# Optimization experiments

Measured on AMD Instinct MI355X. Metric: run time of the kernel, lower is better.

## Reference

```python
import jax, jax.numpy as jnp
import numpy as np

B, T = 64, 512
VOCAB, E, H = 20, 64, 128
D = 2 * H            # 256, bidirectional LSTM output dim
NH, KD = 8, D // 8   # 8 heads, key_dim 32
DU, OUT = 256, 128
NEG = -1e9


def _lstm_scan(x, mask, W, U, b):
    # x: [B,T,E], mask: [B,T] bool. Keras gate order: i, f, g(c), o.
    Bb = x.shape[0]
    Hh = U.shape[0]
    def step(carry, inp):
        h, c = carry
        xt, mt = inp                      # [B,E], [B]
        z = xt @ W + h @ U + b            # [B,4H]
        i, f, g, o = jnp.split(z, 4, axis=-1)
        c_new = jax.nn.sigmoid(f) * c + jax.nn.sigmoid(i) * jnp.tanh(g)
        h_new = jax.nn.sigmoid(o) * jnp.tanh(c_new)
        m = mt[:, None]
        h = jnp.where(m, h_new, h)        # freeze state/output on masked steps
        c = jnp.where(m, c_new, c)
        return (h, c), h
    h0 = jnp.zeros((Bb, Hh), x.dtype)
    _, ys = jax.lax.scan(step, (h0, h0), (jnp.swapaxes(x, 0, 1), mask.T))
    return jnp.swapaxes(ys, 0, 1)         # [B,T,H]


def setup_inputs() -> dict:
    key = jax.random.key(0)
    ks = jax.random.split(key, 24)
    g = lambda k, shape, s: (jax.random.normal(k, shape, jnp.float32) * s)
    inp = {
        'sequences': jax.random.randint(ks[0], (B, T), 0, VOCAB),
        'emb': g(ks[1], (VOCAB, E), 0.05),
        # forward LSTM
        'Wf': g(ks[2], (E, 4 * H), 0.05), 'Uf': g(ks[3], (H, 4 * H), 0.05), 'bf': jnp.zeros((4 * H,), jnp.float32),
        # backward LSTM
        'Wb': g(ks[4], (E, 4 * H), 0.05), 'Ub': g(ks[5], (H, 4 * H), 0.05), 'bb': jnp.zeros((4 * H,), jnp.float32),
        # MHA projections
        'Wq': g(ks[6], (D, NH, KD), 0.05), 'bq': jnp.zeros((NH, KD), jnp.float32),
        'Wk': g(ks[7], (D, NH, KD), 0.05), 'bk': jnp.zeros((NH, KD), jnp.float32),
        'Wv': g(ks[8], (D, NH, KD), 0.05), 'bv': jnp.zeros((NH, KD), jnp.float32),
        'Wo': g(ks[9], (NH, KD, D), 0.05), 'bo': jnp.zeros((D,), jnp.float32),
        # MLP head (input is concat of avg+max pool -> 2*D)
        'W1': g(ks[10], (2 * D, DU), 0.05), 'b1': jnp.zeros((DU,), jnp.float32),
        'W2': g(ks[11], (DU, DU // 2), 0.05), 'b2': jnp.zeros((DU // 2,), jnp.float32),
        'W3': g(ks[12], (DU // 2, OUT), 0.05), 'b3': jnp.zeros((OUT,), jnp.float32),
    }
    return inp


def _forward(sequences, emb, Wf, Uf, bf, Wb, Ub, bb, Wq, bq, Wk, bk, Wv, bv, Wo, bo, W1, b1, W2, b2, W3, b3):
    mask = sequences != 0                       # mask_zero=True
    x = emb[sequences]                          # [B,T,E]
    fwd = _lstm_scan(x, mask, Wf, Uf, bf)
    bwd = _lstm_scan(x[:, ::-1], mask[:, ::-1], Wb, Ub, bb)[:, ::-1]
    h = jnp.concatenate([fwd, bwd], axis=-1)    # [B,T,D]
    # Multi-head self-attention (key-masked, Keras MHA math)
    q = jnp.einsum('btd,dhk->bthk', h, Wq) + bq
    k = jnp.einsum('btd,dhk->bthk', h, Wk) + bk
    v = jnp.einsum('btd,dhk->bthk', h, Wv) + bv
    scores = jnp.einsum('bthk,bshk->bhts', q, k) / jnp.sqrt(jnp.float32(KD))
    scores = jnp.where(mask[:, None, None, :], scores, NEG)
    attn = jax.nn.softmax(scores, axis=-1)      # [B,H,T,T]
    ctx = jnp.einsum('bhts,bshk->bthk', attn, v)
    att = jnp.einsum('bthk,hkd->btd', ctx, Wo) + bo   # [B,T,D]
    # dual pooling (masked mean + masked max)
    mf = mask[..., None].astype(att.dtype)
    avg = (att * mf).sum(axis=1) / jnp.maximum(mf.sum(axis=1), 1.0)
    mx = jnp.where(mask[..., None], att, NEG).max(axis=1)
    p = jnp.concatenate([avg, mx], axis=-1)     # [B,2D]
    x1 = jax.nn.relu(p @ W1 + b1)
    x2 = jax.nn.relu(x1 @ W2 + b2)
    return x2 @ W3 + b3                         # [B,OUT]


def reference(sequences, emb, Wf, Uf, bf, Wb, Ub, bb, Wq, bq, Wk, bk, Wv, bv, Wo, bo, W1, b1, W2, b2, W3, b3):
    return _forward(sequences, emb, Wf, Uf, bf, Wb, Ub, bb, Wq, bq, Wk, bk, Wv, bv, Wo, bo, W1, b1, W2, b2, W3, b3)
```

## Files before the change

kernel.cpp:

```cpp
#include <hip/hip_runtime.h>
#include <math.h>

#define B_ 64
#define T_ 512
#define E_ 64
#define H_ 128
#define NH_ 8
#define KD_ 32
#define BT_ (B_ * T_)
#define NEG_ -1e9f

__device__ __forceinline__ float sigmoidf_(float x) {
    return 1.f / (1.f + __expf(-x));
}
__device__ __forceinline__ float tanhf_(float x) {
    return 1.f - 2.f / (1.f + __expf(2.f * x));
}

template <bool GATHER>
__global__ __launch_bounds__(256, 3) void gemm_f32(
    const float* __restrict__ A, const int* __restrict__ gidx,
    const float* __restrict__ emb, const float* __restrict__ Bm,
    const float* __restrict__ bias, float* __restrict__ C,
    int M, int N, int K)
{
    __shared__ __align__(16) float As[16][132];
    __shared__ __align__(16) float Bs[16][128];
    const int tid = threadIdx.x;
    const int tx = tid & 15, ty = tid >> 4;
    const int ntn = N >> 7;
    const int bm = blockIdx.x / ntn, bn = blockIdx.x % ntn;
    const int m0 = bm << 7, n0 = bn << 7;

    float acc[8][8];
#pragma unroll
    for (int i = 0; i < 8; ++i)
#pragma unroll
        for (int j = 0; j < 8; ++j) acc[i][j] = 0.f;

    const int ac4 = (tid & 3) << 2;
    const int ar  = tid >> 2;
    const int bc4 = (tid & 31) << 2;
    const int br  = tid >> 5;

    for (int k0 = 0; k0 < K; k0 += 16) {
        __syncthreads();
#pragma unroll
        for (int p = 0; p < 2; ++p) {
            const int r = ar + p * 64;
            const int gm = m0 + r;
            const float* src = GATHER
                ? (emb + (size_t)gidx[gm] * K + (k0 + ac4))
                : (A + (size_t)gm * K + (k0 + ac4));
            float4 v = *(const float4*)src;
            As[ac4 + 0][r] = v.x; As[ac4 + 1][r] = v.y;
            As[ac4 + 2][r] = v.z; As[ac4 + 3][r] = v.w;
        }
#pragma unroll
        for (int p = 0; p < 2; ++p) {
            const int rr = br + p * 8;
            float4 v = *(const float4*)(Bm + (size_t)(k0 + rr) * N + (n0 + bc4));
            *(float4*)&Bs[rr][bc4] = v;
        }
        __syncthreads();
#pragma unroll
        for (int k = 0; k < 16; ++k) {
            float a[8], b[8];
            *(float4*)&a[0] = *(const float4*)&As[k][ty << 3];
            *(float4*)&a[4] = *(const float4*)&As[k][(ty << 3) + 4];
            *(float4*)&b[0] = *(const float4*)&Bs[k][tx << 3];
            *(float4*)&b[4] = *(const float4*)&Bs[k][(tx << 3) + 4];
#pragma unroll
            for (int i = 0; i < 8; ++i)
#pragma unroll
                for (int j = 0; j < 8; ++j)
                    acc[i][j] = fmaf(a[i], b[j], acc[i][j]);
        }
    }

    float bv[8];
#pragma unroll
    for (int j = 0; j < 8; ++j) bv[j] = bias[n0 + (tx << 3) + j];
#pragma unroll
    for (int i = 0; i < 8; ++i) {
        float* dst = C + (size_t)(m0 + (ty << 3) + i) * N + n0 + (tx << 3);
        float4 o0 = { acc[i][0] + bv[0], acc[i][1] + bv[1],
                      acc[i][2] + bv[2], acc[i][3] + bv[3] };
        float4 o1 = { acc[i][4] + bv[4], acc[i][5] + bv[5],
                      acc[i][6] + bv[6], acc[i][7] + bv[7] };
        *(float4*)dst = o0;
        *(float4*)(dst + 4) = o1;
    }
}

__global__ __launch_bounds__(512, 2) void lstm_scan(
    const int* __restrict__ seq,
    const float* __restrict__ xwf, const float* __restrict__ xwb,
    const float* __restrict__ Uf, const float* __restrict__ Ub,
    float* __restrict__ hcat)
{
    const int w = blockIdx.x;
    const int dir = w & 1, b = w >> 1;
    const float* xw = dir ? xwb : xwf;
    const float* U  = dir ? Ub  : Uf;
    const int j = threadIdx.x;

    __shared__ __align__(16) float h_lds[128];
    __shared__ float z_lds[512];

    float u[128];
#pragma unroll
    for (int k = 0; k < 128; ++k) u[k] = U[k * 512 + j];
    if (j < 128) h_lds[j] = 0.f;
    float c_reg = 0.f;

    const int* sq = seq + b * T_;
    const float* xr = xw + (size_t)b * T_ * 512;
    float* ho = hcat + (size_t)b * T_ * 256 + dir * 128;
    __syncthreads();

    for (int t = 0; t < T_; ++t) {
        const int te = dir ? (T_ - 1 - t) : t;
        float a0 = xr[(size_t)te * 512 + j];
        float a1 = 0.f, a2 = 0.f, a3 = 0.f;
#pragma unroll
        for (int k = 0; k < 128; k += 4) {
            float4 h4 = *(const float4*)&h_lds[k];
            a0 = fmaf(h4.x, u[k],     a0);
            a1 = fmaf(h4.y, u[k + 1], a1);
            a2 = fmaf(h4.z, u[k + 2], a2);
            a3 = fmaf(h4.w, u[k + 3], a3);
        }
        const float zv = (a0 + a1) + (a2 + a3);
        const float val = (j >= 256 && j < 384) ? tanhf_(zv) : sigmoidf_(zv);
        z_lds[j] = val;
        __syncthreads();
        if (j < 128) {
            const float iv = z_lds[j], fv = z_lds[128 + j];
            const float gv = z_lds[256 + j], ov = z_lds[384 + j];
            const float cn = fmaf(fv, c_reg, iv * gv);
            const float hn = ov * tanhf_(cn);
            const bool mt = (sq[te] != 0);
            const float hprev = h_lds[j];
            const float hout = mt ? hn : hprev;
            c_reg = mt ? cn : c_reg;
            h_lds[j] = hout;
            ho[(size_t)te * 256 + j] = hout;
        }
        __syncthreads();
    }
}

__global__ __launch_bounds__(256, 2) void attn_fused(
    const int* __restrict__ seq,
    const float* __restrict__ q, const float* __restrict__ kk,
    const float* __restrict__ vv, float* __restrict__ ctx)
{
    const int wg = blockIdx.x;
    const int b = wg >> 3, h = wg & 7;
    const int tid = threadIdx.x;

    __shared__ __align__(16) float Ks[16][32];
    __shared__ __align__(16) float Vs[16][32];
    __shared__ float mk[16];

    float qA[32], qB[32];
    {
        const float* qp  = q + (((size_t)(b * T_) + tid) * NH_ + h) * KD_;
        const float* qp2 = qp + (size_t)256 * NH_ * KD_;
#pragma unroll
        for (int k = 0; k < 32; k += 4) {
            float4 v0 = *(const float4*)(qp + k);
            float4 v1 = *(const float4*)(qp2 + k);
            qA[k] = v0.x; qA[k + 1] = v0.y; qA[k + 2] = v0.z; qA[k + 3] = v0.w;
            qB[k] = v1.x; qB[k + 1] = v1.y; qB[k + 2] = v1.z; qB[k + 3] = v1.w;
        }
    }
    float ctxA[32], ctxB[32];
#pragma unroll
    for (int k = 0; k < 32; ++k) { ctxA[k] = 0.f; ctxB[k] = 0.f; }
    float mA = -1e30f, mB = -1e30f, lA = 0.f, lB = 0.f;

    const int lr = (tid & 127) >> 3;
    const int lc = (tid & 7) << 2;
    const bool loadV = (tid >= 128);

    for (int c = 0; c < T_ / 16; ++c) {
        const int s0 = c << 4;
        __syncthreads();
        {
            const float* src = (loadV ? vv : kk) +
                (((size_t)(b * T_) + s0 + lr) * NH_ + h) * KD_ + lc;
            float4 v = *(const float4*)src;
            if (loadV) *(float4*)&Vs[lr][lc] = v;
            else       *(float4*)&Ks[lr][lc] = v;
            if (tid < 16) mk[tid] = (seq[b * T_ + s0 + tid] != 0) ? 0.f : 1.f;
        }
        __syncthreads();

        float sA[16], sB[16];
#pragma unroll
        for (int s = 0; s < 16; ++s) {
            float dA = 0.f, dB = 0.f;
#pragma unroll
            for (int k = 0; k < 32; k += 4) {
                float4 k4 = *(const float4*)&Ks[s][k];
                dA = fmaf(k4.x, qA[k], dA); dA = fmaf(k4.y, qA[k + 1], dA);
                dA = fmaf(k4.z, qA[k + 2], dA); dA = fmaf(k4.w, qA[k + 3], dA);
                dB = fmaf(k4.x, qB[k], dB); dB = fmaf(k4.y, qB[k + 1], dB);
                dB = fmaf(k4.z, qB[k + 2], dB); dB = fmaf(k4.w, qB[k + 3], dB);
            }
            const float SCL = 0.17677669529663687f;
            const bool masked = (mk[s] > 0.5f);
            sA[s] = masked ? NEG_ : dA * SCL;
            sB[s] = masked ? NEG_ : dB * SCL;
        }
        float cmA = sA[0], cmB = sB[0];
#pragma unroll
        for (int s = 1; s < 16; ++s) {
            cmA = fmaxf(cmA, sA[s]); cmB = fmaxf(cmB, sB[s]);
        }
        const float mnA = fmaxf(mA, cmA), mnB = fmaxf(mB, cmB);
        const float alA = __expf(mA - mnA), alB = __expf(mB - mnB);
        float psA = 0.f, psB = 0.f;
#pragma unroll
        for (int s = 0; s < 16; ++s) {
            float pa = __expf(sA[s] - mnA); sA[s] = pa; psA += pa;
            float pb = __expf(sB[s] - mnB); sB[s] = pb; psB += pb;
        }
        lA = fmaf(lA, alA, psA); lB = fmaf(lB, alB, psB);
        mA = mnA; mB = mnB;
#pragma unroll
        for (int k = 0; k < 32; ++k) { ctxA[k] *= alA; ctxB[k] *= alB; }
#pragma unroll
        for (int s = 0; s < 16; ++s) {
#pragma unroll
            for (int k = 0; k < 32; k += 4) {
                float4 v4 = *(const float4*)&Vs[s][k];
                ctxA[k]     = fmaf(sA[s], v4.x, ctxA[k]);
                ctxA[k + 1] = fmaf(sA[s], v4.y, ctxA[k + 1]);
                ctxA[k + 2] = fmaf(sA[s], v4.z, ctxA[k + 2]);
                ctxA[k + 3] = fmaf(sA[s], v4.w, ctxA[k + 3]);
                ctxB[k]     = fmaf(sB[s], v4.x, ctxB[k]);
                ctxB[k + 1] = fmaf(sB[s], v4.y, ctxB[k + 1]);
                ctxB[k + 2] = fmaf(sB[s], v4.z, ctxB[k + 2]);
                ctxB[k + 3] = fmaf(sB[s], v4.w, ctxB[k + 3]);
            }
        }
    }

    const float iA = 1.f / lA, iB = 1.f / lB;
    float* dA_ = ctx + (((size_t)(b * T_) + tid) * NH_ + h) * KD_;
    float* dB_ = dA_ + (size_t)256 * NH_ * KD_;
#pragma unroll
    for (int k = 0; k < 32; k += 4) {
        float4 o0 = { ctxA[k] * iA, ctxA[k + 1] * iA,
                      ctxA[k + 2] * iA, ctxA[k + 3] * iA };
        float4 o1 = { ctxB[k] * iB, ctxB[k + 1] * iB,
                      ctxB[k + 2] * iB, ctxB[k + 3] * iB };
        *(float4*)(dA_ + k) = o0;
        *(float4*)(dB_ + k) = o1;
    }
}

__global__ void pool_kernel(const int* __restrict__ seq,
                            const float* __restrict__ att,
                            float* __restrict__ p)
{
    const int b = blockIdx.x;
    const int d = threadIdx.x;
    __shared__ float mk[T_];
    for (int t = d; t < T_; t += 256)
        mk[t] = (seq[b * T_ + t] != 0) ? 1.f : 0.f;
    __syncthreads();
    float sum = 0.f, mx = NEG_, cnt = 0.f;
    for (int t = 0; t < T_; ++t) {
        const float a = att[((size_t)b * T_ + t) * 256 + d];
        const float m = mk[t];
        cnt += m;
        sum = fmaf(m, a, sum);
        mx = fmaxf(mx, (m > 0.5f) ? a : NEG_);
    }
    p[b * 512 + d] = sum / fmaxf(cnt, 1.f);
    p[b * 512 + 256 + d] = mx;
}

__global__ void mlp_kernel(const float* __restrict__ p,
                           const float* __restrict__ W1, const float* __restrict__ b1,
                           const float* __restrict__ W2, const float* __restrict__ b2,
                           const float* __restrict__ W3, const float* __restrict__ b3,
                           float* __restrict__ out)
{
    const int b = blockIdx.x;
    const int tid = threadIdx.x;
    __shared__ float pl[512];
    __shared__ float x1l[256];
    __shared__ float x2l[128];
    pl[tid] = p[b * 512 + tid];
    pl[tid + 256] = p[b * 512 + 256 + tid];
    __syncthreads();
    {
        float acc = b1[tid];
        for (int k = 0; k < 512; ++k) acc = fmaf(pl[k], W1[k * 256 + tid], acc);
        x1l[tid] = fmaxf(acc, 0.f);
    }
    __syncthreads();
    if (tid < 128) {
        float acc = b2[tid];
        for (int k = 0; k < 256; ++k) acc = fmaf(x1l[k], W2[k * 128 + tid], acc);
        x2l[tid] = fmaxf(acc, 0.f);
    }
    __syncthreads();
    if (tid < 128) {
        float acc = b3[tid];
        for (int k = 0; k < 128; ++k) acc = fmaf(x2l[k], W3[k * 128 + tid], acc);
        out[b * 128 + tid] = acc;
    }
}

extern "C" void kernel_launch(void* const* d_in, const int* in_sizes, int n_in,
                              void* d_out, int out_size, void* d_ws, size_t ws_size,
                              hipStream_t stream)
{
    (void)in_sizes; (void)n_in; (void)out_size; (void)ws_size;
    const int*   seq = (const int*)d_in[0];
    const float* emb = (const float*)d_in[1];
    const float* Wf  = (const float*)d_in[2];
    const float* Uf  = (const float*)d_in[3];
    const float* bf  = (const float*)d_in[4];
    const float* Wb  = (const float*)d_in[5];
    const float* Ub  = (const float*)d_in[6];
    const float* bb  = (const float*)d_in[7];
    const float* Wq  = (const float*)d_in[8];
    const float* bq  = (const float*)d_in[9];
    const float* Wk  = (const float*)d_in[10];
    const float* bk  = (const float*)d_in[11];
    const float* Wv  = (const float*)d_in[12];
    const float* bv  = (const float*)d_in[13];
    const float* Wo  = (const float*)d_in[14];
    const float* bo  = (const float*)d_in[15];
    const float* W1  = (const float*)d_in[16];
    const float* b1  = (const float*)d_in[17];
    const float* W2  = (const float*)d_in[18];
    const float* b2  = (const float*)d_in[19];
    const float* W3  = (const float*)d_in[20];
    const float* b3  = (const float*)d_in[21];
    float* out = (float*)d_out;
    float* ws  = (float*)d_ws;

    float* xw_f = ws;
    float* xw_b = ws + 16777216;
    float* hcat = ws + 33554432;
    float* qb   = ws;
    float* kb   = ws + 8388608;
    float* vb   = ws + 16777216;
    float* cxb  = ws + 25165824;
    float* attb = ws + 33554432;
    float* pb   = ws + 41943040;

    const dim3 blk256(256), blk512(512);

    gemm_f32<true><<<dim3((BT_ / 128) * (512 / 128)), blk256, 0, stream>>>(
        nullptr, seq, emb, Wf, bf, xw_f, BT_, 512, 64);
    gemm_f32<true><<<dim3((BT_ / 128) * (512 / 128)), blk256, 0, stream>>>(
        nullptr, seq, emb, Wb, bb, xw_b, BT_, 512, 64);

    lstm_scan<<<dim3(128), blk512, 0, stream>>>(seq, xw_f, xw_b, Uf, Ub, hcat);

    gemm_f32<false><<<dim3((BT_ / 128) * (256 / 128)), blk256, 0, stream>>>(
        hcat, nullptr, nullptr, Wq, bq, qb, BT_, 256, 256);
    gemm_f32<false><<<dim3((BT_ / 128) * (256 / 128)), blk256, 0, stream>>>(
        hcat, nullptr, nullptr, Wk, bk, kb, BT_, 256, 256);
    gemm_f32<false><<<dim3((BT_ / 128) * (256 / 128)), blk256, 0, stream>>>(
        hcat, nullptr, nullptr, Wv, bv, vb, BT_, 256, 256);

    attn_fused<<<dim3(B_ * NH_), blk256, 0, stream>>>(seq, qb, kb, vb, cxb);

    gemm_f32<false><<<dim3((BT_ / 128) * (256 / 128)), blk256, 0, stream>>>(
        cxb, nullptr, nullptr, Wo, bo, attb, BT_, 256, 256);

    pool_kernel<<<dim3(B_), blk256, 0, stream>>>(seq, attb, pb);
    mlp_kernel<<<dim3(B_), blk256, 0, stream>>>(pb, W1, b1, W2, b2, W3, b3, out);
}
```

Before: 1.073 ms.

## Restructure LSTM scan with split-K DPP reduction and single barrier per step

The input-projection GEMM now writes gate columns interleaved (i,f,g,o per hidden unit), so each LSTM thread can read all four gate pre-activations for its unit as one float4. The scan assigns 4 threads per hidden unit, each holding a 32-wide K slice of all four gates in registers. Partial sums are reduced with DPP quad swaps, and every thread then computes the cell update redundantly. A double-buffered h in LDS removes the second barrier and the z_lds exchange, and the next step's xw is prefetched one iteration ahead. This targets the per-step latency of the serial recurrence, but it costs strided, uncoalesced B loads in the permuted GEMM.

```diff
diff --git a/kernel.cpp b/kernel.cpp
--- a/kernel.cpp
+++ b/kernel.cpp
@@ -17,7 +17,14 @@
     return 1.f - 2.f / (1.f + __expf(2.f * x));
 }
 
-template <bool GATHER>
+__device__ __forceinline__ float qswap1(float x) {
+    return __int_as_float(__builtin_amdgcn_mov_dpp(__float_as_int(x), 0xB1, 0xF, 0xF, true));
+}
+__device__ __forceinline__ float qswap2(float x) {
+    return __int_as_float(__builtin_amdgcn_mov_dpp(__float_as_int(x), 0x4E, 0xF, 0xF, true));
+}
+
+template <bool GATHER, bool PERM>
 __global__ __launch_bounds__(256, 3) void gemm_f32(
     const float* __restrict__ A, const int* __restrict__ gidx,
     const float* __restrict__ emb, const float* __restrict__ Bm,
@@ -59,8 +66,17 @@
 #pragma unroll
         for (int p = 0; p < 2; ++p) {
             const int rr = br + p * 8;
-            float4 v = *(const float4*)(Bm + (size_t)(k0 + rr) * N + (n0 + bc4));
-            *(float4*)&Bs[rr][bc4] = v;
+            if (PERM) {
+                const float* brow = Bm + (size_t)(k0 + rr) * N;
+                const int base = (n0 >> 2) + (tid & 31);
+                Bs[rr][bc4 + 0] = brow[base];
+                Bs[rr][bc4 + 1] = brow[128 + base];
+                Bs[rr][bc4 + 2] = brow[256 + base];
+                Bs[rr][bc4 + 3] = brow[384 + base];
+            } else {
+                float4 v = *(const float4*)(Bm + (size_t)(k0 + rr) * N + (n0 + bc4));
+                *(float4*)&Bs[rr][bc4] = v;
+            }
         }
         __syncthreads();
 #pragma unroll
@@ -80,7 +96,10 @@
 
     float bv[8];
 #pragma unroll
-    for (int j = 0; j < 8; ++j) bv[j] = bias[n0 + (tx << 3) + j];
+    for (int j = 0; j < 8; ++j) {
+        const int n = n0 + (tx << 3) + j;
+        bv[j] = PERM ? bias[((n & 3) << 7) + (n >> 2)] : bias[n];
+    }
 #pragma unroll
     for (int i = 0; i < 8; ++i) {
         float* dst = C + (size_t)(m0 + (ty << 3) + i) * N + n0 + (tx << 3);
@@ -103,51 +122,74 @@
     const int dir = w & 1, b = w >> 1;
     const float* xw = dir ? xwb : xwf;
     const float* U  = dir ? Ub  : Uf;
-    const int j = threadIdx.x;
-
-    __shared__ __align__(16) float h_lds[128];
-    __shared__ float z_lds[512];
-
-    float u[128];
-#pragma unroll
-    for (int k = 0; k < 128; ++k) u[k] = U[k * 512 + j];
-    if (j < 128) h_lds[j] = 0.f;
-    float c_reg = 0.f;
-
-    const int* sq = seq + b * T_;
+    const int tid = threadIdx.x;
+    const int jj = tid >> 2, ks = tid & 3;
+
+    __shared__ __align__(16) float hbuf[2][4][36];
+    __shared__ float mkl[T_];
+
+    float u[4][32];
+#pragma unroll
+    for (int g = 0; g < 4; ++g)
+#pragma unroll
+        for (int kk = 0; kk < 32; ++kk)
+            u[g][kk] = U[(size_t)(32 * ks + kk) * 512 + g * 128 + jj];
+#pragma unroll
+    for (int g = 0; g < 4; ++g)
+#pragma unroll
+        for (int kk = 0; kk < 32; ++kk)
+            asm volatile("" : "+v"(u[g][kk]));
+
+    mkl[tid] = (seq[b * T_ + tid] != 0) ? 1.f : 0.f;
+    if (tid < 2 * 4 * 36) ((float*)hbuf)[tid] = 0.f;
+
+    float h_cur = 0.f, c_cur = 0.f;
+    float* ho = hcat + (size_t)b * T_ * 256 + dir * 128;
     const float* xr = xw + (size_t)b * T_ * 512;
-    float* ho = hcat + (size_t)b * T_ * 256 + dir * 128;
+
     __syncthreads();
 
+    int te = dir ? (T_ - 1) : 0;
+    float4 xwv = *(const float4*)&xr[(size_t)te * 512 + jj * 4];
+
+    int p = 0;
     for (int t = 0; t < T_; ++t) {
-        const int te = dir ? (T_ - 1 - t) : t;
-        float a0 = xr[(size_t)te * 512 + j];
-        float a1 = 0.f, a2 = 0.f, a3 = 0.f;
-#pragma unroll
-        for (int k = 0; k < 128; k += 4) {
-            float4 h4 = *(const float4*)&h_lds[k];
-            a0 = fmaf(h4.x, u[k],     a0);
-            a1 = fmaf(h4.y, u[k + 1], a1);
-            a2 = fmaf(h4.z, u[k + 2], a2);
-            a3 = fmaf(h4.w, u[k + 3], a3);
-        }
-        const float zv = (a0 + a1) + (a2 + a3);
-        const float val = (j >= 256 && j < 384) ? tanhf_(zv) : sigmoidf_(zv);
-        z_lds[j] = val;
+        const int te_n  = dir ? (te - 1) : (te + 1);
+        const int te_pf = (t == T_ - 1) ? te : te_n;
+        const float4 xw_n = *(const float4*)&xr[(size_t)te_pf * 512 + jj * 4];
+
+        float a0 = 0.f, a1 = 0.f, a2 = 0.f, a3 = 0.f;
+        const float* hc = hbuf[p][ks];
+#pragma unroll
+        for (int c = 0; c < 8; ++c) {
+            const float4 h4 = *(const float4*)&hc[c * 4];
+            a0 = fmaf(h4.x, u[0][c*4+0], a0); a0 = fmaf(h4.y, u[0][c*4+1], a0);
+            a0 = fmaf(h4.z, u[0][c*4+2], a0); a0 = fmaf(h4.w, u[0][c*4+3], a0);
+            a1 = fmaf(h4.x, u[1][c*4+0], a1); a1 = fmaf(h4.y, u[1][c*4+1], a1);
+            a1 = fmaf(h4.z, u[1][c*4+2], a1); a1 = fmaf(h4.w, u[1][c*4+3], a1);
+            a2 = fmaf(h4.x, u[2][c*4+0], a2); a2 = fmaf(h4.y, u[2][c*4+1], a2);
+            a2 = fmaf(h4.z, u[2][c*4+2], a2); a2 = fmaf(h4.w, u[2][c*4+3], a2);
+            a3 = fmaf(h4.x, u[3][c*4+0], a3); a3 = fmaf(h4.y, u[3][c*4+1], a3);
+            a3 = fmaf(h4.z, u[3][c*4+2], a3); a3 = fmaf(h4.w, u[3][c*4+3], a3);
+        }
+        a0 += qswap1(a0); a0 += qswap2(a0);
+        a1 += qswap1(a1); a1 += qswap2(a1);
+        a2 += qswap1(a2); a2 += qswap2(a2);
+        a3 += qswap1(a3); a3 += qswap2(a3);
+
+        const float zi = xwv.x + a0, zf = xwv.y + a1;
+        const float zg = xwv.z + a2, zo = xwv.w + a3;
+        const float cn = fmaf(sigmoidf_(zf), c_cur, sigmoidf_(zi) * tanhf_(zg));
+        const float hn = sigmoidf_(zo) * tanhf_(cn);
+        const float m  = mkl[te];
+        const float hm = (m > 0.5f) ? hn : h_cur;
+        c_cur = (m > 0.5f) ? cn : c_cur;
+        h_cur = hm;
+
+        if ((jj >> 5) == ks) hbuf[1 - p][ks][jj & 31] = hm;
+        if (ks == 0) ho[(size_t)te * 256 + jj] = hm;
         __syncthreads();
-        if (j < 128) {
-            const float iv = z_lds[j], fv = z_lds[128 + j];
-            const float gv = z_lds[256 + j], ov = z_lds[384 + j];
-            const float cn = fmaf(fv, c_reg, iv * gv);
-            const float hn = ov * tanhf_(cn);
-            const bool mt = (sq[te] != 0);
-            const float hprev = h_lds[j];
-            const float hout = mt ? hn : hprev;
-            c_reg = mt ? cn : c_reg;
-            h_lds[j] = hout;
-            ho[(size_t)te * 256 + j] = hout;
-        }
-        __syncthreads();
+        p ^= 1; te = te_n; xwv = xw_n;
     }
 }
 
@@ -360,23 +402,23 @@
 
     const dim3 blk256(256), blk512(512);
 
-    gemm_f32<true><<<dim3((BT_ / 128) * (512 / 128)), blk256, 0, stream>>>(
+    gemm_f32<true, true><<<dim3((BT_ / 128) * (512 / 128)), blk256, 0, stream>>>(
         nullptr, seq, emb, Wf, bf, xw_f, BT_, 512, 64);
-    gemm_f32<true><<<dim3((BT_ / 128) * (512 / 128)), blk256, 0, stream>>>(
+    gemm_f32<true, true><<<dim3((BT_ / 128) * (512 / 128)), blk256, 0, stream>>>(
         nullptr, seq, emb, Wb, bb, xw_b, BT_, 512, 64);
 
     lstm_scan<<<dim3(128), blk512, 0, stream>>>(seq, xw_f, xw_b, Uf, Ub, hcat);
 
-    gemm_f32<false><<<dim3((BT_ / 128) * (256 / 128)), blk256, 0, stream>>>(
+    gemm_f32<false, false><<<dim3((BT_ / 128) * (256 / 128)), blk256, 0, stream>>>(
         hcat, nullptr, nullptr, Wq, bq, qb, BT_, 256, 256);
-    gemm_f32<false><<<dim3((BT_ / 128) * (256 / 128)), blk256, 0, stream>>>(
+    gemm_f32<false, false><<<dim3((BT_ / 128) * (256 / 128)), blk256, 0, stream>>>(
         hcat, nullptr, nullptr, Wk, bk, kb, BT_, 256, 256);
-    gemm_f32<false><<<dim3((BT_ / 128) * (256 / 128)), blk256, 0, stream>>>(
+    gemm_f32<false, false><<<dim3((BT_ / 128) * (256 / 128)), blk256, 0, stream>>>(
         hcat, nullptr, nullptr, Wv, bv, vb, BT_, 256, 256);
 
     attn_fused<<<dim3(B_ * NH_), blk256, 0, stream>>>(seq, qb, kb, vb, cxb);
 
-    gemm_f32<false><<<dim3((BT_ / 128) * (256 / 128)), blk256, 0, stream>>>(
+    gemm_f32<false, false><<<dim3((BT_ / 128) * (256 / 128)), blk256, 0, stream>>>(
         cxb, nullptr, nullptr, Wo, bo, attb, BT_, 256, 256);
 
     pool_kernel<<<dim3(B_), blk256, 0, stream>>>(seq, attb, pb);
```

Measured after the change: 985.8 us. -8.1%, faster.
